# Optimization experiments

Measured on AMD Instinct MI355X. Metric: run time of the kernel, lower is better.

The kernel has to match this reference:

```python
import jax, jax.numpy as jnp
import numpy as np

VOCAB, D = 500000, 128
B, K = 16384, 10          # word-level pairs, negatives per pair
B2, L, W = 8192, 5, 10    # mwe batch, max entity len, 2*window context


def setup_inputs() -> dict:
    key = jax.random.key(0)
    ks = jax.random.split(key, 9)
    scale = 1.0 / np.sqrt(D)
    return {
        "center_table": jax.random.normal(ks[0], (VOCAB, D), jnp.float32) * scale,
        "context_table": jax.random.normal(ks[1], (VOCAB, D), jnp.float32) * scale,
        "w_center": jax.random.randint(ks[2], (B,), 0, VOCAB),
        "w_outside": jax.random.randint(ks[3], (B,), 0, VOCAB),
        "w_neg": jax.random.randint(ks[4], (B, K), 0, VOCAB),
        "m_center": jax.random.randint(ks[5], (B2, L), 0, VOCAB),
        "m_len": jax.random.randint(ks[6], (B2,), 1, L + 1),
        "m_outside": jax.random.randint(ks[7], (B2, W), 0, VOCAB),
        "m_neg": jax.random.randint(ks[8], (B2 * W, K), 0, VOCAB),
    }


def _masked_mean_mwe(emb, lengths):
    # emb: (B2, L, D); masked mean over first `lengths` tokens (mwe_f)
    mask = (jnp.arange(emb.shape[1])[None, :] < lengths[:, None]).astype(emb.dtype)
    return jnp.sum(emb * mask[:, :, None], axis=1) / lengths[:, None].astype(emb.dtype)


def reference(center_table, context_table, w_center, w_outside, w_neg,
              m_center, m_len, m_outside, m_neg):
    ls = jax.nn.log_sigmoid

    # ----- word-level skip-gram negative sampling -----
    ce = center_table[w_center]            # (B, D)
    oe = context_table[w_outside]          # (B, D)
    ne = context_table[w_neg]              # (B, K, D)
    pos = -ls(jnp.sum(oe * ce, axis=-1))                       # (B,)
    neg = jnp.sum(-ls(-jnp.einsum('bkd,bd->bk', ne, ce)), -1)  # (B,)
    loss_words = jnp.mean(pos + neg)

    # ----- MWE skip-gram negative sampling -----
    valid = (m_outside.reshape(-1) != 0)                       # pad token == 0
    mwe = _masked_mean_mwe(center_table[m_center], m_len)      # (B2, D)
    mwe_rep = jnp.broadcast_to(mwe[:, None, :], (B2, W, D)).reshape(-1, D)  # (B2*W, D)
    oe2 = context_table[m_outside.reshape(-1)]                 # (B2*W, D)
    ne2 = context_table[m_neg]                                 # (B2*W, K, D)
    pos2 = -ls(jnp.sum(oe2 * mwe_rep, axis=-1))                           # (B2*W,)
    neg2 = jnp.sum(-ls(-jnp.einsum('nkd,nd->nk', ne2, mwe_rep)), -1)      # (B2*W,)
    vf = valid.astype(pos2.dtype)
    loss_mwes = jnp.sum((pos2 + neg2) * vf) / jnp.maximum(jnp.sum(vf), 1.0)

    return loss_words + 25.0 * loss_mwes
```

## Files before the change

### kernel.cpp

```cpp
#include <hip/hip_runtime.h>
#include <hip/hip_bf16.h>
#include <math.h>

#define DIMD 128
#define NB    16384
#define NK    10
#define NB2   8192
#define NL    5
#define NW    10
#define PPW   4
#define NBLK_M (NB2 / 4)
#define NBLK_W (NB / (4 * PPW))
#define NBLK   (NBLK_M + NBLK_W)

__device__ __forceinline__ float softplus_fast(float z) {
  return fmaxf(z, 0.0f) + __logf(1.0f + __expf(-fabsf(z)));
}

__device__ __forceinline__ float4 ld4(const float* __restrict__ p) {
  return *reinterpret_cast<const float4*>(p);
}

__device__ __forceinline__ float rs8(float v[8], int lane) {
  const bool b4 = (lane & 16) != 0, b3 = (lane & 8) != 0, b2 = (lane & 4) != 0;
#pragma unroll
  for (int j = 0; j < 4; ++j) {
    float recv = __shfl_xor(b4 ? v[j] : v[j + 4], 16);
    v[j] = (b4 ? v[j + 4] : v[j]) + recv;
  }
#pragma unroll
  for (int j = 0; j < 2; ++j) {
    float recv = __shfl_xor(b3 ? v[j] : v[j + 2], 8);
    v[j] = (b3 ? v[j + 2] : v[j]) + recv;
  }
  float recv = __shfl_xor(b2 ? v[0] : v[1], 4);
  float s = (b2 ? v[1] : v[0]) + recv;
  s += __shfl_xor(s, 2);
  s += __shfl_xor(s, 1);
  return s;
}

__device__ __forceinline__ float window_term(
    const float* __restrict__ xtq, float4 c4, int pos,
    const int* __restrict__ nrow, int lane, int h, float zsgn, float wmask) {
  const int2 n01 = *reinterpret_cast<const int2*>(nrow + 0);
  const int2 n23 = *reinterpret_cast<const int2*>(nrow + 2);
  const int2 n45 = *reinterpret_cast<const int2*>(nrow + 4);
  const int2 n67 = *reinterpret_cast<const int2*>(nrow + 6);
  const int2 n89 = *reinterpret_cast<const int2*>(nrow + 8);
  const int i0 = h ? n01.x : pos;
  const int i1 = h ? n23.x : n01.y;
  const int i2 = h ? n45.x : n23.y;
  const int i3 = h ? n67.x : n45.y;
  const int i4 = h ? n89.x : n67.y;
  const int i5 = n89.y;
  const float4 r0 = ld4(xtq + (size_t)i0 * DIMD);
  const float4 r1 = ld4(xtq + (size_t)i1 * DIMD);
  const float4 r2 = ld4(xtq + (size_t)i2 * DIMD);
  const float4 r3 = ld4(xtq + (size_t)i3 * DIMD);
  const float4 r4 = ld4(xtq + (size_t)i4 * DIMD);
  const float4 r5 = ld4(xtq + (size_t)i5 * DIMD);
  float v[8];
  v[0] = c4.x * r0.x + c4.y * r0.y + c4.z * r0.z + c4.w * r0.w;
  v[1] = c4.x * r1.x + c4.y * r1.y + c4.z * r1.z + c4.w * r1.w;
  v[2] = c4.x * r2.x + c4.y * r2.y + c4.z * r2.z + c4.w * r2.w;
  v[3] = c4.x * r3.x + c4.y * r3.y + c4.z * r3.z + c4.w * r3.w;
  v[4] = c4.x * r4.x + c4.y * r4.y + c4.z * r4.z + c4.w * r4.w;
  v[5] = c4.x * r5.x + c4.y * r5.y + c4.z * r5.z + c4.w * r5.w;
  v[6] = 0.0f; v[7] = 0.0f;
  const float s = rs8(v, lane);
  return softplus_fast(s * zsgn) * wmask;
}

__global__ __launch_bounds__(256) void k_main(
    const float* __restrict__ ct, const float* __restrict__ xt,
    const int* __restrict__ wc, const int* __restrict__ wo,
    const int* __restrict__ wn,
    const int* __restrict__ mc, const int* __restrict__ mlen,
    const int* __restrict__ mo, const int* __restrict__ mn,
    float2* __restrict__ partials) {
  const int bid  = blockIdx.x;
  const int widx = threadIdx.x >> 6;
  const int lane = threadIdx.x & 63;
  const int q = lane & 31, h = lane >> 5;
  const int idx3 = ((lane >> 4) & 1) * 4 + ((lane >> 3) & 1) * 2 + ((lane >> 2) & 1);
  const bool vld = (idx3 < 5) || (idx3 == 5 && h == 0);
  const float zsgn  = (idx3 == 0 && h == 0) ? -1.0f : 1.0f;
  const float wmask = (((lane & 3) == 0) && vld) ? 1.0f : 0.0f;
  const float* __restrict__ xtq = xt + q * 4;
  const float* __restrict__ ctq = ct + q * 4;

  float acc = 0.0f, cnt = 0.0f;

  if (bid < NBLK_M) {
    const int g = bid * 4 + widx;
    const int len = mlen[g];
    int ti[NL];
#pragma unroll
    for (int t = 0; t < NL; ++t) ti[t] = mc[g * NL + t];
    float4 m = make_float4(0.0f, 0.0f, 0.0f, 0.0f);
#pragma unroll
    for (int t = 0; t < NL; ++t) {
      const float4 e = ld4(ctq + (size_t)ti[t] * DIMD);
      if (t < len) { m.x += e.x; m.y += e.y; m.z += e.z; m.w += e.w; }
    }
    const float inv = 1.0f / (float)len;
    m.x *= inv; m.y *= inv; m.z *= inv; m.w *= inv;

    int ov[NW];
#pragma unroll
    for (int j = 0; j < NW; j += 2) {
      const int2 o2 = *reinterpret_cast<const int2*>(mo + g * NW + j);
      ov[j] = o2.x; ov[j + 1] = o2.y;
    }
#pragma unroll
    for (int w = 0; w < NW; ++w) {
      const int o = ov[w];
      if (o == 0) continue;
      acc += window_term(xtq, m, o, mn + (size_t)(g * NW + w) * NK,
                         lane, h, zsgn, wmask);
      cnt += 1.0f;
    }
  } else {
    const int ww = (bid - NBLK_M) * 4 + widx;
#pragma unroll
    for (int p = 0; p < PPW; ++p) {
      const int b = ww * PPW + p;
      const float4 c4 = ld4(ctq + (size_t)wc[b] * DIMD);
      acc += window_term(xtq, c4, wo[b], wn + (size_t)b * NK,
                         lane, h, zsgn, wmask);
    }
  }

  acc += __shfl_xor(acc, 4);
  acc += __shfl_xor(acc, 8);
  acc += __shfl_xor(acc, 16);
  acc += __shfl_xor(acc, 32);

  __shared__ float sm[4], sc[4];
  if (lane == 0) { sm[widx] = acc; sc[widx] = cnt; }
  __syncthreads();
  if (threadIdx.x == 0)
    partials[bid] = make_float2((sm[0] + sm[1]) + (sm[2] + sm[3]),
                                (sc[0] + sc[1]) + (sc[2] + sc[3]));
}

__global__ __launch_bounds__(256) void k_final(
    const float2* __restrict__ partials, float* __restrict__ out) {
  __shared__ float sa[256], sb[256], sc[256];
  float S = 0.0f, MS = 0.0f, MC = 0.0f;
  for (int i = threadIdx.x; i < NBLK_M; i += 256) {
    const float2 v = partials[i];
    MS += v.x; MC += v.y;
  }
  for (int i = NBLK_M + threadIdx.x; i < NBLK; i += 256) S += partials[i].x;
  sa[threadIdx.x] = S; sb[threadIdx.x] = MS; sc[threadIdx.x] = MC;
  __syncthreads();
  if (threadIdx.x == 0) {
    float s = 0.0f, ms = 0.0f, mc2 = 0.0f;
    for (int i = 0; i < 256; ++i) { s += sa[i]; ms += sb[i]; mc2 += sc[i]; }
    out[0] = s / (float)NB + 25.0f * (ms / fmaxf(mc2, 1.0f));
  }
}

extern "C" void kernel_launch(void* const* d_in, const int* in_sizes, int n_in,
                              void* d_out, int out_size, void* d_ws, size_t ws_size,
                              hipStream_t stream) {
  const float* ct   = (const float*)d_in[0];
  const float* xt   = (const float*)d_in[1];
  const int*   wc   = (const int*)d_in[2];
  const int*   wo   = (const int*)d_in[3];
  const int*   wn   = (const int*)d_in[4];
  const int*   mc   = (const int*)d_in[5];
  const int*   mlen = (const int*)d_in[6];
  const int*   mo   = (const int*)d_in[7];
  const int*   mn   = (const int*)d_in[8];

  float2* partials = (float2*)d_ws;

  k_main<<<NBLK, 256, 0, stream>>>(ct, xt, wc, wo, wn, mc, mlen, mo, mn, partials);
  k_final<<<1, 256, 0, stream>>>(partials, (float*)d_out);
}
```

Before: 94.05 us.

## Split window gathers into issue/reduce phases, pair windows, and shuffle-reduce final

The per-window gather-and-reduce is split into a load-issue phase and a reduce phase. Two windows (or two word pairs) are issued back to back before either is reduced, which raises memory-level parallelism for the random row gathers. The MWE loop no longer branches on pad tokens: it always gathers and masks the result, so it may do extra loads for padded windows. The final reduction replaces a serial 256-element shared-memory loop with wave shuffles. The trade-off is higher register pressure from holding twelve float4 rows at once.

Measured after the change: 91.24 us. 1.03x faster.

```diff
diff --git a/kernel.cpp b/kernel.cpp
--- a/kernel.cpp
+++ b/kernel.cpp
@@ -40,9 +40,9 @@
   return s;
 }
 
-__device__ __forceinline__ float window_term(
-    const float* __restrict__ xtq, float4 c4, int pos,
-    const int* __restrict__ nrow, int lane, int h, float zsgn, float wmask) {
+__device__ __forceinline__ void win_issue(
+    const float* __restrict__ xtq, int pos, const int* __restrict__ nrow,
+    int h, float4 r[6]) {
   const int2 n01 = *reinterpret_cast<const int2*>(nrow + 0);
   const int2 n23 = *reinterpret_cast<const int2*>(nrow + 2);
   const int2 n45 = *reinterpret_cast<const int2*>(nrow + 4);
@@ -54,19 +54,20 @@
   const int i3 = h ? n67.x : n45.y;
   const int i4 = h ? n89.x : n67.y;
   const int i5 = n89.y;
-  const float4 r0 = ld4(xtq + (size_t)i0 * DIMD);
-  const float4 r1 = ld4(xtq + (size_t)i1 * DIMD);
-  const float4 r2 = ld4(xtq + (size_t)i2 * DIMD);
-  const float4 r3 = ld4(xtq + (size_t)i3 * DIMD);
-  const float4 r4 = ld4(xtq + (size_t)i4 * DIMD);
-  const float4 r5 = ld4(xtq + (size_t)i5 * DIMD);
+  r[0] = ld4(xtq + (size_t)i0 * DIMD);
+  r[1] = ld4(xtq + (size_t)i1 * DIMD);
+  r[2] = ld4(xtq + (size_t)i2 * DIMD);
+  r[3] = ld4(xtq + (size_t)i3 * DIMD);
+  r[4] = ld4(xtq + (size_t)i4 * DIMD);
+  r[5] = ld4(xtq + (size_t)i5 * DIMD);
+}
+
+__device__ __forceinline__ float win_reduce(
+    const float4 r[6], float4 c4, int lane, float zsgn, float wmask) {
   float v[8];
-  v[0] = c4.x * r0.x + c4.y * r0.y + c4.z * r0.z + c4.w * r0.w;
-  v[1] = c4.x * r1.x + c4.y * r1.y + c4.z * r1.z + c4.w * r1.w;
-  v[2] = c4.x * r2.x + c4.y * r2.y + c4.z * r2.z + c4.w * r2.w;
-  v[3] = c4.x * r3.x + c4.y * r3.y + c4.z * r3.z + c4.w * r3.w;
-  v[4] = c4.x * r4.x + c4.y * r4.y + c4.z * r4.z + c4.w * r4.w;
-  v[5] = c4.x * r5.x + c4.y * r5.y + c4.z * r5.z + c4.w * r5.w;
+#pragma unroll
+  for (int s = 0; s < 6; ++s)
+    v[s] = c4.x * r[s].x + c4.y * r[s].y + c4.z * r[s].z + c4.w * r[s].w;
   v[6] = 0.0f; v[7] = 0.0f;
   const float s = rs8(v, lane);
   return softplus_fast(s * zsgn) * wmask;
@@ -113,22 +114,32 @@
       const int2 o2 = *reinterpret_cast<const int2*>(mo + g * NW + j);
       ov[j] = o2.x; ov[j + 1] = o2.y;
     }
-#pragma unroll
-    for (int w = 0; w < NW; ++w) {
-      const int o = ov[w];
-      if (o == 0) continue;
-      acc += window_term(xtq, m, o, mn + (size_t)(g * NW + w) * NK,
-                         lane, h, zsgn, wmask);
-      cnt += 1.0f;
+    const int* __restrict__ mng = mn + (size_t)g * NW * NK;
+#pragma unroll
+    for (int w = 0; w < NW; w += 2) {
+      const int oa = ov[w], ob = ov[w + 1];
+      const float vfa = (oa != 0) ? 1.0f : 0.0f;
+      const float vfb = (ob != 0) ? 1.0f : 0.0f;
+      float4 ra[6], rb[6];
+      win_issue(xtq, oa, mng + (size_t)w * NK, h, ra);
+      win_issue(xtq, ob, mng + (size_t)(w + 1) * NK, h, rb);
+      const float ta = win_reduce(ra, m, lane, zsgn, wmask);
+      const float tb = win_reduce(rb, m, lane, zsgn, wmask);
+      acc += ta * vfa + tb * vfb;
+      cnt += vfa + vfb;
     }
   } else {
     const int ww = (bid - NBLK_M) * 4 + widx;
 #pragma unroll
-    for (int p = 0; p < PPW; ++p) {
-      const int b = ww * PPW + p;
-      const float4 c4 = ld4(ctq + (size_t)wc[b] * DIMD);
-      acc += window_term(xtq, c4, wo[b], wn + (size_t)b * NK,
-                         lane, h, zsgn, wmask);
+    for (int p = 0; p < PPW; p += 2) {
+      const int b0 = ww * PPW + p, b1 = b0 + 1;
+      const float4 ca = ld4(ctq + (size_t)wc[b0] * DIMD);
+      const float4 cb = ld4(ctq + (size_t)wc[b1] * DIMD);
+      float4 ra[6], rb[6];
+      win_issue(xtq, wo[b0], wn + (size_t)b0 * NK, h, ra);
+      win_issue(xtq, wo[b1], wn + (size_t)b1 * NK, h, rb);
+      acc += win_reduce(ra, ca, lane, zsgn, wmask);
+      acc += win_reduce(rb, cb, lane, zsgn, wmask);
     }
   }
 
@@ -147,18 +158,24 @@
 
 __global__ __launch_bounds__(256) void k_final(
     const float2* __restrict__ partials, float* __restrict__ out) {
-  __shared__ float sa[256], sb[256], sc[256];
+  const int widx = threadIdx.x >> 6, lane = threadIdx.x & 63;
   float S = 0.0f, MS = 0.0f, MC = 0.0f;
   for (int i = threadIdx.x; i < NBLK_M; i += 256) {
     const float2 v = partials[i];
     MS += v.x; MC += v.y;
   }
   for (int i = NBLK_M + threadIdx.x; i < NBLK; i += 256) S += partials[i].x;
-  sa[threadIdx.x] = S; sb[threadIdx.x] = MS; sc[threadIdx.x] = MC;
+#pragma unroll
+  for (int d = 32; d >= 1; d >>= 1) {
+    S += __shfl_xor(S, d); MS += __shfl_xor(MS, d); MC += __shfl_xor(MC, d);
+  }
+  __shared__ float sa[4], sb[4], sc[4];
+  if (lane == 0) { sa[widx] = S; sb[widx] = MS; sc[widx] = MC; }
   __syncthreads();
   if (threadIdx.x == 0) {
-    float s = 0.0f, ms = 0.0f, mc2 = 0.0f;
-    for (int i = 0; i < 256; ++i) { s += sa[i]; ms += sb[i]; mc2 += sc[i]; }
+    const float s   = (sa[0] + sa[1]) + (sa[2] + sa[3]);
+    const float ms  = (sb[0] + sb[1]) + (sb[2] + sb[3]);
+    const float mc2 = (sc[0] + sc[1]) + (sc[2] + sc[3]);
     out[0] = s / (float)NB + 25.0f * (ms / fmaxf(mc2, 1.0f));
   }
 }
```
